# Kernel tuning notes

Measured on AMD Instinct MI355X. Metric: run time of the kernel, lower is better.

The kernel has to match this reference:

```python
import jax, jax.numpy as jnp
import numpy as np

NUM_HEADS = 12
NUM_GROUPS = 4
LN_EPS = 1e-12
NEG = -10000.0


def _ln(x, g, b):
    m = x.mean(-1, keepdims=True)
    v = ((x - m) ** 2).mean(-1, keepdims=True)
    return (x - m) * jax.lax.rsqrt(v + LN_EPS) * g + b


def _attention(h, ext_mask, Wattn, battn, ln):
    # h: [B,S,H]; ext_mask additive [B,1,1,S]; Wattn [4,H,H] = (q,k,v,o); battn [4,H]; ln [2,H]
    B, S, H = h.shape
    dh = H // NUM_HEADS
    q = (h @ Wattn[0] + battn[0]).reshape(B, S, NUM_HEADS, dh)
    k = (h @ Wattn[1] + battn[1]).reshape(B, S, NUM_HEADS, dh)
    v = (h @ Wattn[2] + battn[2]).reshape(B, S, NUM_HEADS, dh)
    scores = jnp.einsum('bqhd,bkhd->bhqk', q, k) * (1.0 / np.sqrt(dh)) + ext_mask
    p = jax.nn.softmax(scores, axis=-1)
    ctx = jnp.einsum('bhqk,bkhd->bqhd', p, v).reshape(B, S, H)
    # BertSelfOutput: dense + residual + LayerNorm
    return _ln(ctx @ Wattn[3] + battn[3] + h, ln[0], ln[1])


def _ffn(x, Wi, bi, Wo, bo, ln):
    # BertIntermediate (gelu) + BertOutput (dense + residual + LayerNorm)
    return _ln(jax.nn.gelu(x @ Wi + bi, approximate=False) @ Wo + bo + x, ln[0], ln[1])


def _bert_layer(h, ext_mask, Wattn, battn, ln_attn, Wi, bi, Wo, bo, ln_out):
    a = _attention(h, ext_mask, Wattn, battn, ln_attn)
    return _ffn(a, Wi, bi, Wo, bo, ln_out)


def _hier_attention(h, hier_mask, Wattn, battn, ln_attn, Wi, bi, Wo, bo, ln_out):
    # group masks [G,B,S]: 1 where hier_mask == group_id (ids 1..G)
    gids = jnp.arange(1, NUM_GROUPS + 1)
    masks = (hier_mask[None] == gids[:, None, None]).astype(h.dtype)  # [G,B,S]
    ext = (1.0 - masks)[:, :, None, None, :] * NEG                    # [G,B,1,1,S]
    # one full BertLayer per group (vectorized over G instead of batch concat)
    outs = jax.vmap(lambda m: _bert_layer(h, m, Wattn, battn, ln_attn, Wi, bi, Wo, bo, ln_out))(ext)  # [G,B,S,H]
    return jnp.sum(outs * masks[..., None], axis=0)


def reference(hidden_states, attention_mask, main_Wattn, main_battn, main_ln_attn,
              main_Wi, main_bi, main_Wo, main_bo, main_ln_out,
              hier_Wattn, hier_battn, hier_ln_attn, hier_Wi, hier_bi, hier_Wo,
              hier_bo, hier_ln_out, hier_mask):
    attn_out = _attention(hidden_states, attention_mask, main_Wattn, main_battn, main_ln_attn)
    hier_out = _hier_attention(hidden_states, hier_mask, hier_Wattn, hier_battn,
                               hier_ln_attn, hier_Wi, hier_bi, hier_Wo, hier_bo, hier_ln_out)
    combined = attn_out + hier_out
    return _ffn(combined, main_Wi, main_bi, main_Wo, main_bo, main_ln_out)


def setup_inputs() -> dict:
    key = jax.random.key(0)
    ks = jax.random.split(key, 20)
    B, S, H, F = 8, 512, 768, 3072
    W = 0.02  # weight init scale

    def layer_params(k):
        kk = jax.random.split(k, 8)
        return dict(
            Wattn=jax.random.normal(kk[0], (4, H, H), jnp.float32) * W,
            battn=jax.random.normal(kk[1], (4, H), jnp.float32) * W,
            ln_attn=jnp.stack([1.0 + jax.random.normal(kk[2], (H,), jnp.float32) * W,
                               jax.random.normal(kk[3], (H,), jnp.float32) * W]),
            Wi=jax.random.normal(kk[4], (H, F), jnp.float32) * W,
            bi=jax.random.normal(kk[5], (F,), jnp.float32) * W,
            Wo=jax.random.normal(kk[6], (F, H), jnp.float32) * W,
            bo=jax.random.normal(kk[7], (H,), jnp.float32) * W,
            ln_out=jnp.stack([1.0 + jax.random.normal(kk[2], (H,), jnp.float32) * W,
                              jax.random.normal(kk[3], (H,), jnp.float32) * W]),
        )

    main = layer_params(ks[0])
    hier = layer_params(ks[1])
    inp = {
        'hidden_states': jax.random.normal(ks[2], (B, S, H), jnp.float32),
        'attention_mask': jnp.zeros((B, 1, 1, S), jnp.float32),
        'hier_mask': jax.random.randint(ks[3], (B, S), 0, 5).astype(jnp.int64),
    }
    for name, p in (('main', main), ('hier', hier)):
        for k2, v in p.items():
            inp[f'{name}_{k2}'] = v
    return inp
```

## Files before the change

kernel.cpp:

```cpp
#include <hip/hip_runtime.h>
#include <hip/hip_bf16.h>

#define DI __device__ __forceinline__

typedef __attribute__((ext_vector_type(4))) float  f32x4;
typedef __attribute__((ext_vector_type(8))) short  s16x8;
typedef __attribute__((ext_vector_type(4))) short  s16x4;
typedef __attribute__((ext_vector_type(8))) __bf16 bf16x8;

DI short f2bf(float f) {
  union { float f; unsigned u; } v; v.f = f;
  unsigned r = v.u + 0x7fffu + ((v.u >> 16) & 1u);
  return (short)(r >> 16);
}

DI f32x4 mfma16(s16x8 a, s16x8 b, f32x4 c) {
  return __builtin_amdgcn_mfma_f32_16x16x32_bf16(
      __builtin_bit_cast(bf16x8, a), __builtin_bit_cast(bf16x8, b), c, 0, 0, 0);
}

typedef const __attribute__((address_space(1))) unsigned* gas_p;
typedef __attribute__((address_space(3))) unsigned* las_p;
DI void gload16(const void* g, void* l) {
  __builtin_amdgcn_global_load_lds((gas_p)g, (las_p)l, 16, 0, 0);
}

template<int N> DI void wait_vmcnt() {
  asm volatile("s_waitcnt vmcnt(%0)" :: "n"(N) : "memory");
}

__global__ __launch_bounds__(256) void cast_bf16(const float* __restrict__ x,
                                                 short* __restrict__ y) {
  const int i = (blockIdx.x * 256 + threadIdx.x) * 4;
  const float4 t = *(const float4*)&x[i];
  s16x4 o;
  o[0] = f2bf(t.x); o[1] = f2bf(t.y); o[2] = f2bf(t.z); o[3] = f2bf(t.w);
  *(s16x4*)&y[i] = o;
}

struct TJob { const float* src; short* dst; int K, N, tile0; };
struct TJobs { TJob j[12]; };

__global__ __launch_bounds__(256) void transpose_w(TJobs jobs) {
  __shared__ float T[32][33];
  const int t = blockIdx.x;
  int ji = 0;
#pragma unroll
  for (int i = 1; i < 12; ++i) if (jobs.j[i].tile0 <= t) ji = i;
  const float* src = jobs.j[ji].src;
  short* dst = jobs.j[ji].dst;
  const int K = jobs.j[ji].K, N = jobs.j[ji].N;
  const int lt = t - jobs.j[ji].tile0;
  const int tn = N >> 5;
  const int n0 = (lt % tn) << 5, k0 = (lt / tn) << 5;
  const int tid = threadIdx.x;
#pragma unroll
  for (int i = 0; i < 4; ++i) {
    const int c = i * 256 + tid, r = c >> 5, cc = c & 31;
    T[cc][r] = src[(long long)(k0 + r) * N + n0 + cc];
  }
  __syncthreads();
#pragma unroll
  for (int i = 0; i < 4; ++i) {
    const int c = i * 256 + tid, r = c >> 5, cc = c & 31;
    dst[(long long)(n0 + r) * K + k0 + cc] = f2bf(T[r][cc]);
  }
}

template<int BM, int BN, int WM, int WN, int EPI>
__global__ __launch_bounds__(256) void gemm_bt(
    const short* __restrict__ A, int lda, long long sA,
    const short* __restrict__ B, int ldb, long long sB,
    void* __restrict__ Cv, int ldc,
    long long cOuter, int cInner, int cStride,
    const float* __restrict__ bias,
    int K, int nSplit,
    short* __restrict__ vtOut) {
  constexpr int BK = 32;
  constexpr int WNW = BN / WN;
  constexpr int MFR = WM / 16, NFR = WN / 16;
  constexpr int ALD = BM / 64;
  constexpr int BLD = BN / 64;
  constexpr int LPT = ALD + BLD;

  __shared__ short As[3][BM * BK];
  __shared__ short Bs[3][BN * BK];

  const int z = blockIdx.z;
  const int zb = z / nSplit, zs = z - zb * nSplit;
  const short* Ab = A + (long long)zb * sA + (long long)zs * K;
  const short* Bb = B + (long long)zb * sB + (long long)zs * K;
  const long long cOff = (long long)(z / cInner) * cOuter + (long long)(z % cInner) * cStride;

  const int bm = blockIdx.x * BM;
  const int bn = blockIdx.y * BN;
  const int tid = threadIdx.x;
  const int wave = tid >> 6, lane = tid & 63;
  const int wm = (wave / WNW) * WM;
  const int wn = (wave % WNW) * WN;
  const int l16 = lane & 15, lk = lane >> 4;

  const int scol = ((tid & 3) ^ ((tid >> 3) & 3)) * 8;
  const short* aBase = Ab + (long long)(bm + (tid >> 2)) * lda + scol;
  const short* bBase = Bb + (long long)(bn + (tid >> 2)) * ldb + scol;
  const int ldsOff = wave * 64 * 8;
  const int rslot = (lk ^ ((l16 >> 1) & 3)) * 8;

  f32x4 acc[MFR][NFR] = {};

  auto stage = [&](int buf, int kt) {
#pragma unroll
    for (int i = 0; i < ALD; ++i)
      gload16(aBase + kt + (long long)(i * 64) * lda, &As[buf][i * 2048 + ldsOff]);
#pragma unroll
    for (int i = 0; i < BLD; ++i)
      gload16(bBase + kt + (long long)(i * 64) * ldb, &Bs[buf][i * 2048 + ldsOff]);
  };

  const int nt = K / BK;
  stage(0, 0);
  if (nt > 1) stage(1, BK);
  int cur = 0;
  for (int t = 0; t < nt; ++t) {
    if (t + 1 < nt) wait_vmcnt<LPT>();
    else            wait_vmcnt<0>();
    __builtin_amdgcn_s_barrier();
    s16x8 af[MFR], bfr[NFR];
#pragma unroll
    for (int mi = 0; mi < MFR; ++mi)
      af[mi] = *(const s16x8*)&As[cur][(wm + mi * 16 + l16) * BK + rslot];
#pragma unroll
    for (int ni = 0; ni < NFR; ++ni)
      bfr[ni] = *(const s16x8*)&Bs[cur][(wn + ni * 16 + l16) * BK + rslot];
#pragma unroll
    for (int mi = 0; mi < MFR; ++mi)
#pragma unroll
      for (int ni = 0; ni < NFR; ++ni)
        acc[mi][ni] = mfma16(bfr[ni], af[mi], acc[mi][ni]);
    if (t + 2 < nt) {
      const int nb = cur + 2 >= 3 ? cur - 1 : cur + 2;
      stage(nb, (t + 2) * BK);
    }
    cur = (cur + 1 == 3) ? 0 : cur + 1;
  }

#pragma unroll
  for (int mi = 0; mi < MFR; ++mi) {
    const int row = bm + wm + mi * 16 + l16;
#pragma unroll
    for (int ni = 0; ni < NFR; ++ni) {
      const int col = bn + wn + ni * 16 + lk * 4;
      const long long idx = cOff + (long long)row * ldc + col;
      f32x4 bv = {};
      if (EPI != 2 && bias) bv = *(const f32x4*)&bias[col];
      f32x4 v = acc[mi][ni] + bv;
      if constexpr (EPI == 0 || EPI == 3) {
        s16x4 o;
#pragma unroll
        for (int r = 0; r < 4; ++r) o[r] = f2bf(v[r]);
        *(s16x4*)&((short*)Cv)[idx] = o;
        if constexpr (EPI == 3) {
          if (col >= 1536) {
            const int b = row >> 9, s = row & 511;
            const int hc = col - 1536;
            const int bh = b * 12 + (hc >> 6);
            const int d0 = hc & 63;
            short* vp = vtOut + (long long)bh * 32768 + (long long)d0 * 512 + s;
#pragma unroll
            for (int r = 0; r < 4; ++r) vp[r * 512] = o[r];
          }
        }
      } else if constexpr (EPI == 1) {
        s16x4 o;
#pragma unroll
        for (int r = 0; r < 4; ++r) {
          const float g = 0.5f * v[r] * (1.f + erff(v[r] * 0.70710678118654752f));
          o[r] = f2bf(g);
        }
        *(s16x4*)&((short*)Cv)[idx] = o;
      } else {
        *(f32x4*)&((float*)Cv)[idx] = v;
      }
    }
  }
}

template<int HIER>
__global__ __launch_bounds__(256) void attn_scores(
    const short* __restrict__ QKV,
    const float* __restrict__ amask,
    const int* __restrict__ hmask,
    short* __restrict__ P) {
  __shared__ short Qs[32 * 64];
  __shared__ short Ks[256 * 64];
  __shared__ float red[32 * 4];
  __shared__ int   hm[512];

  const int bh = blockIdx.y;
  const int b = bh / 12, hh = bh % 12;
  const int q0 = blockIdx.x * 32;
  const int tid = threadIdx.x;
  const int wave = tid >> 6, lane = tid & 63;
  const int l16 = lane & 15, lk = lane >> 4;
  const long long rowbase = (long long)(b * 512) * 2304 + hh * 64;

  {
    const int c = tid;
    const int d8 = ((c & 7) ^ ((c >> 3) & 7)) * 8;
    gload16(QKV + rowbase + (long long)(q0 + (c >> 3)) * 2304 + d8,
            &Qs[wave * 64 * 8]);
  }
  if constexpr (HIER) {
    for (int i = tid; i < 512; i += 256) hm[i] = hmask[b * 512 + i];
  }

  f32x4 acc[2][8] = {};
#pragma unroll
  for (int kc = 0; kc < 2; ++kc) {
    if (kc) __syncthreads();
#pragma unroll
    for (int i = 0; i < 8; ++i) {
      const int c = i * 256 + tid;
      const int d8 = ((c & 7) ^ ((c >> 3) & 7)) * 8;
      gload16(QKV + rowbase + 768 + (long long)(kc * 256 + (c >> 3)) * 2304 + d8,
              &Ks[(i * 256 + wave * 64) * 8]);
    }
    __syncthreads();
#pragma unroll
    for (int ks = 0; ks < 2; ++ks) {
      s16x8 af[2], bfr[4];
#pragma unroll
      for (int mi = 0; mi < 2; ++mi)
        af[mi] = *(const s16x8*)&Qs[(mi * 16 + l16) * 64 +
                                    (((ks * 4 + lk) ^ (l16 & 7)) * 8)];
#pragma unroll
      for (int ni = 0; ni < 4; ++ni)
        bfr[ni] = *(const s16x8*)&Ks[(wave * 64 + ni * 16 + l16) * 64 +
                                     (((ks * 4 + lk) ^ (l16 & 7)) * 8)];
#pragma unroll
      for (int mi = 0; mi < 2; ++mi)
#pragma unroll
        for (int ni = 0; ni < 4; ++ni)
          acc[mi][kc * 4 + ni] = mfma16(af[mi], bfr[ni], acc[mi][kc * 4 + ni]);
    }
  }

  int gq[2][4];
  if constexpr (HIER) {
#pragma unroll
    for (int mi = 0; mi < 2; ++mi)
#pragma unroll
      for (int r = 0; r < 4; ++r)
        gq[mi][r] = hm[q0 + mi * 16 + lk * 4 + r];
  }
  int hk[8]; float am[8];
#pragma unroll
  for (int nig = 0; nig < 8; ++nig) {
    const int col = (nig >> 2) * 256 + wave * 64 + (nig & 3) * 16 + l16;
    if constexpr (HIER) hk[nig] = hm[col];
    else                am[nig] = amask[b * 512 + col];
  }
#pragma unroll
  for (int mi = 0; mi < 2; ++mi)
#pragma unroll
    for (int nig = 0; nig < 8; ++nig)
#pragma unroll
      for (int r = 0; r < 4; ++r) {
        float v = acc[mi][nig][r] * 0.125f;
        if constexpr (HIER) v += (hk[nig] == gq[mi][r]) ? 0.f : -10000.f;
        else                v += am[nig];
        acc[mi][nig][r] = v;
      }

  float mx[2][4];
#pragma unroll
  for (int mi = 0; mi < 2; ++mi)
#pragma unroll
    for (int r = 0; r < 4; ++r) {
      float m = acc[mi][0][r];
#pragma unroll
      for (int nig = 1; nig < 8; ++nig) m = fmaxf(m, acc[mi][nig][r]);
#pragma unroll
      for (int d = 1; d < 16; d <<= 1) m = fmaxf(m, __shfl_xor(m, d));
      mx[mi][r] = m;
      red[(mi * 16 + lk * 4 + r) * 4 + wave] = m;
    }
  __syncthreads();
#pragma unroll
  for (int mi = 0; mi < 2; ++mi)
#pragma unroll
    for (int r = 0; r < 4; ++r) {
      const int q = mi * 16 + lk * 4 + r;
      mx[mi][r] = fmaxf(fmaxf(red[q * 4], red[q * 4 + 1]),
                        fmaxf(red[q * 4 + 2], red[q * 4 + 3]));
    }
  __syncthreads();

  float sm[2][4];
#pragma unroll
  for (int mi = 0; mi < 2; ++mi)
#pragma unroll
    for (int r = 0; r < 4; ++r) {
      float s = 0.f;
#pragma unroll
      for (int nig = 0; nig < 8; ++nig) {
        const float e = __expf(acc[mi][nig][r] - mx[mi][r]);
        acc[mi][nig][r] = e;
        s += e;
      }
#pragma unroll
      for (int d = 1; d < 16; d <<= 1) s += __shfl_xor(s, d);
      sm[mi][r] = s;
      red[(mi * 16 + lk * 4 + r) * 4 + wave] = s;
    }
  __syncthreads();
#pragma unroll
  for (int mi = 0; mi < 2; ++mi)
#pragma unroll
    for (int r = 0; r < 4; ++r) {
      const int q = mi * 16 + lk * 4 + r;
      sm[mi][r] = 1.f / (red[q * 4] + red[q * 4 + 1] + red[q * 4 + 2] + red[q * 4 + 3]);
    }

  const long long Pbase = (long long)bh * 512 * 512;
#pragma unroll
  for (int mi = 0; mi < 2; ++mi)
#pragma unroll
    for (int nig = 0; nig < 8; ++nig) {
      const int col = (nig >> 2) * 256 + wave * 64 + (nig & 3) * 16 + l16;
#pragma unroll
      for (int r = 0; r < 4; ++r) {
        const int q = mi * 16 + lk * 4 + r;
        P[Pbase + (long long)(q0 + q) * 512 + col] = f2bf(acc[mi][nig][r] * sm[mi][r]);
      }
    }
}

template<int NS, int MODE>
__global__ __launch_bounds__(256) void ln_red(
    const float* __restrict__ part, const float* __restrict__ bias,
    const float* __restrict__ res, const float* __restrict__ ln,
    float* __restrict__ outf, short* __restrict__ outb,
    const int* __restrict__ hmask) {
  constexpr long long SP = 4096LL * 768;
  const int row = blockIdx.x * 4 + (threadIdx.x >> 6);
  const int lane = threadIdx.x & 63;
  const long long rb = (long long)row * 768;
  float v[12];
  float s = 0.f;
#pragma unroll
  for (int i = 0; i < 3; ++i) {
    const int c4 = lane + (i << 6);
    float4 t = ((const float4*)(res + rb))[c4];
    const float4 bv = ((const float4*)bias)[c4];
    t.x += bv.x; t.y += bv.y; t.z += bv.z; t.w += bv.w;
#pragma unroll
    for (int ss = 0; ss < NS; ++ss) {
      const float4 p = ((const float4*)(part + ss * SP + rb))[c4];
      t.x += p.x; t.y += p.y; t.z += p.z; t.w += p.w;
    }
    v[i * 4 + 0] = t.x; v[i * 4 + 1] = t.y; v[i * 4 + 2] = t.z; v[i * 4 + 3] = t.w;
    s += t.x + t.y + t.z + t.w;
  }
#pragma unroll
  for (int d = 1; d < 64; d <<= 1) s += __shfl_xor(s, d);
  const float mean = s * (1.f / 768.f);
  float vs = 0.f;
#pragma unroll
  for (int i = 0; i < 12; ++i) { const float dv = v[i] - mean; vs += dv * dv; }
#pragma unroll
  for (int d = 1; d < 64; d <<= 1) vs += __shfl_xor(vs, d);
  const float rstd = rsqrtf(vs * (1.f / 768.f) + 1e-12f);
  int keep = 1;
  if constexpr (MODE == 2) keep = (hmask[row] != 0);
#pragma unroll
  for (int i = 0; i < 3; ++i) {
    const int c4 = lane + (i << 6);
    const float4 g = ((const float4*)ln)[c4];
    const float4 be = ((const float4*)(ln + 768))[c4];
    const float gg[4] = {g.x, g.y, g.z, g.w}, bb[4] = {be.x, be.y, be.z, be.w};
    float resv[4];
#pragma unroll
    for (int j = 0; j < 4; ++j) {
      float yv = (v[i * 4 + j] - mean) * rstd * gg[j] + bb[j];
      if constexpr (MODE == 2) {
        const float a = outf[rb + c4 * 4 + j];
        yv = a + (keep ? yv : 0.f);
      }
      resv[j] = yv;
    }
    float4 of; of.x = resv[0]; of.y = resv[1]; of.z = resv[2]; of.w = resv[3];
    ((float4*)(outf + rb))[c4] = of;
    if constexpr (MODE >= 1) {
      s16x4 ob;
#pragma unroll
      for (int j = 0; j < 4; ++j) ob[j] = f2bf(resv[j]);
      *(s16x4*)&outb[rb + c4 * 4] = ob;
    }
  }
}

extern "C" void kernel_launch(void* const* d_in, const int* in_sizes, int n_in,
                              void* d_out, int out_size, void* d_ws, size_t ws_size,
                              hipStream_t stream) {
  (void)in_sizes; (void)n_in; (void)out_size; (void)ws_size;
  const float* h      = (const float*)d_in[0];
  const float* amask  = (const float*)d_in[1];
  const int*   hmask  = (const int*)d_in[2];
  const float* mWattn = (const float*)d_in[3];
  const float* mbattn = (const float*)d_in[4];
  const float* mlnA   = (const float*)d_in[5];
  const float* mWi    = (const float*)d_in[6];
  const float* mbi    = (const float*)d_in[7];
  const float* mWo    = (const float*)d_in[8];
  const float* mbo    = (const float*)d_in[9];
  const float* mlnO   = (const float*)d_in[10];
  const float* hWattn = (const float*)d_in[11];
  const float* hbattn = (const float*)d_in[12];
  const float* hlnA   = (const float*)d_in[13];
  const float* hWi    = (const float*)d_in[14];
  const float* hbi    = (const float*)d_in[15];
  const float* hWo    = (const float*)d_in[16];
  const float* hbo    = (const float*)d_in[17];
  const float* hlnO   = (const float*)d_in[18];
  float* out = (float*)d_out;

  char* ws = (char*)d_ws;
  size_t off = 0;
  auto alloc = [&](size_t bytes) {
    void* p = ws + off;
    off += (bytes + 255) & ~(size_t)255;
    return p;
  };
  short* wq_m = (short*)alloc(2304ull * 768 * 2);
  short* wq_h = (short*)alloc(2304ull * 768 * 2);
  short* wo2  = (short*)alloc(2ull * 768 * 768 * 2);
  short* wi_m = (short*)alloc(3072ull * 768 * 2);
  short* wi_h = (short*)alloc(3072ull * 768 * 2);
  short* wf_m = (short*)alloc(768ull * 3072 * 2);
  short* wf_h = (short*)alloc(768ull * 3072 * 2);
  short* hbf  = (short*)alloc(4096ull * 768 * 2);
  short* qkv  = (short*)alloc(4096ull * 2304 * 2);
  short* vt   = (short*)alloc(96ull * 64 * 512 * 2);
  short* Pb   = (short*)alloc(96ull * 512 * 512 * 2);
  short* ctxb = (short*)alloc(2ull * 4096 * 768 * 2);
  float* pre1 = (float*)alloc(4096ull * 768 * 4);
  float* attn = (float*)alloc(4096ull * 768 * 4);
  short* abf  = (short*)alloc(4096ull * 768 * 2);
  short* cbf  = (short*)alloc(4096ull * 768 * 2);
  short* mid  = qkv;
  float* part = (float*)Pb;

  const long long SC = 4096LL * 768;

  cast_bf16<<<dim3(3072), dim3(256), 0, stream>>>(h, hbf);

  TJobs tj; int tile = 0; int nj = 0;
  auto add = [&](const float* s, short* d, int K, int N) {
    tj.j[nj].src = s; tj.j[nj].dst = d; tj.j[nj].K = K; tj.j[nj].N = N; tj.j[nj].tile0 = tile;
    tile += (K / 32) * (N / 32); nj++;
  };
  add(mWattn,              wq_m,              768, 768);
  add(mWattn + 589824,     wq_m + 589824,     768, 768);
  add(mWattn + 2 * 589824, wq_m + 2 * 589824, 768, 768);
  add(mWattn + 3 * 589824, wo2,               768, 768);
  add(mWi,                 wi_m,              768, 3072);
  add(mWo,                 wf_m,              3072, 768);
  add(hWattn,              wq_h,              768, 768);
  add(hWattn + 589824,     wq_h + 589824,     768, 768);
  add(hWattn + 2 * 589824, wq_h + 2 * 589824, 768, 768);
  add(hWattn + 3 * 589824, wo2 + 589824,      768, 768);
  add(hWi,                 wi_h,              768, 3072);
  add(hWo,                 wf_h,              3072, 768);
  transpose_w<<<dim3(tile), dim3(256), 0, stream>>>(tj);

  auto attn_path = [&](const short* wq, const float* battn, int hier, short* ctx) {
    gemm_bt<128, 128, 64, 64, 3><<<dim3(32, 18, 1), dim3(256), 0, stream>>>(
        hbf, 768, 0, wq, 768, 0, qkv, 2304, 0, 1, 0, battn, 768, 1, vt);
    if (hier)
      attn_scores<1><<<dim3(16, 96), dim3(256), 0, stream>>>(qkv, amask, hmask, Pb);
    else
      attn_scores<0><<<dim3(16, 96), dim3(256), 0, stream>>>(qkv, amask, hmask, Pb);
    gemm_bt<64, 64, 32, 32, 0><<<dim3(8, 1, 96), dim3(256), 0, stream>>>(
        Pb, 512, 262144LL, vt, 512, 32768LL,
        ctx, 768, 512LL * 768, 12, 64, nullptr, 512, 1, nullptr);
  };

  attn_path(wq_m, mbattn, 0, ctxb);
  attn_path(wq_h, hbattn, 1, ctxb + SC);

  gemm_bt<128, 128, 64, 64, 2><<<dim3(32, 6, 4), dim3(256), 0, stream>>>(
      ctxb, 768, SC, wo2, 768, 589824LL, part, 768, SC, 1, 0, nullptr, 384, 2, nullptr);
  ln_red<2, 0><<<dim3(1024), dim3(256), 0, stream>>>(
      part, mbattn + 2304, h, mlnA, attn, nullptr, nullptr);
  ln_red<2, 1><<<dim3(1024), dim3(256), 0, stream>>>(
      part + 2 * SC, hbattn + 2304, h, hlnA, pre1, abf, nullptr);

  gemm_bt<128, 128, 64, 64, 1><<<dim3(32, 24, 1), dim3(256), 0, stream>>>(
      abf, 768, 0, wi_h, 768, 0, mid, 3072, 0, 1, 0, hbi, 768, 1, nullptr);
  gemm_bt<128, 128, 64, 64, 2><<<dim3(32, 6, 4), dim3(256), 0, stream>>>(
      mid, 3072, 0, wf_h, 3072, 0, part, 768, SC, 1, 0, nullptr, 768, 4, nullptr);
  ln_red<4, 2><<<dim3(1024), dim3(256), 0, stream>>>(
      part, hbo, pre1, hlnO, attn, cbf, hmask);

  gemm_bt<128, 128, 64, 64, 1><<<dim3(32, 24, 1), dim3(256), 0, stream>>>(
      cbf, 768, 0, wi_m, 768, 0, mid, 3072, 0, 1, 0, mbi, 768, 1, nullptr);
  gemm_bt<128, 128, 64, 64, 2><<<dim3(32, 6, 4), dim3(256), 0, stream>>>(
      mid, 3072, 0, wf_m, 3072, 0, part, 768, SC, 1, 0, nullptr, 768, 4, nullptr);
  ln_red<4, 0><<<dim3(1024), dim3(256), 0, stream>>>(
      part, mbo, attn, mlnO, out, nullptr, nullptr);
}
```

Measured before the change: 372.3 us.

## Add 2-wave 128x128 GEMM kernel and batch main/hier QKV projections

Adds a new 128-thread GEMM kernel where each of two waves computes a 64x128 sub-tile with double-buffered LDS. It is used for all large projections (QKV, output, FFN up and down) in place of the 256-thread triple-buffered kernel. The main and hierarchical QKV projections are also merged into one batched launch over a z dimension, with per-batch bias selection and a V-transpose output offset. The aim is more register-level reuse per wave and fewer launches, at the cost of higher register pressure, fewer threads per block and a shallower prefetch pipeline.

Result: slower. 525.0 us (+41.0%).

```diff
diff --git a/kernel.cpp b/kernel.cpp
--- a/kernel.cpp
+++ b/kernel.cpp
@@ -67,6 +67,115 @@
   }
 }
 
+template<int EPI>
+__global__ __launch_bounds__(128) void gemm2w(
+    const short* __restrict__ A, int lda, long long sA,
+    const short* __restrict__ B, int ldb, long long sB,
+    void* __restrict__ Cv, int ldc,
+    long long cOuter, int cInner, int cStride,
+    const float* __restrict__ bias, const float* __restrict__ bias2,
+    int K, int nSplit,
+    short* __restrict__ vtOut) {
+  constexpr int BK = 32;
+  __shared__ short As[2][128 * BK];
+  __shared__ short Bs[2][128 * BK];
+
+  const int z = blockIdx.z;
+  const int zb = z / nSplit, zs = z - zb * nSplit;
+  const short* Ab = A + (long long)zb * sA + (long long)zs * K;
+  const short* Bb = B + (long long)zb * sB + (long long)zs * K;
+  const long long cOff = (long long)(z / cInner) * cOuter + (long long)(z % cInner) * cStride;
+  const float* bi = (bias2 && zb) ? bias2 : bias;
+
+  const int bm = blockIdx.x * 128;
+  const int bn = blockIdx.y * 128;
+  const int tid = threadIdx.x;
+  const int wave = tid >> 6, lane = tid & 63;
+  const int l16 = lane & 15, lk = lane >> 4;
+
+  const int scol = ((tid & 3) ^ ((tid >> 3) & 3)) * 8;
+  const short* aBase = Ab + (long long)(bm + (tid >> 2)) * lda + scol;
+  const short* bBase = Bb + (long long)(bn + (tid >> 2)) * ldb + scol;
+  const int ldsOff = wave * 512;
+  const int rslot = (lk ^ ((l16 >> 1) & 3)) * 8;
+
+  f32x4 acc[4][8] = {};
+
+  auto stage = [&](int buf, int kt) {
+#pragma unroll
+    for (int i = 0; i < 4; ++i)
+      gload16(aBase + kt + (long long)(i * 32) * lda, &As[buf][i * 1024 + ldsOff]);
+#pragma unroll
+    for (int i = 0; i < 4; ++i)
+      gload16(bBase + kt + (long long)(i * 32) * ldb, &Bs[buf][i * 1024 + ldsOff]);
+  };
+
+  const int nt = K / BK;
+  stage(0, 0);
+  wait_vmcnt<0>();
+  __builtin_amdgcn_s_barrier();
+  int cur = 0;
+  for (int t = 0; t < nt; ++t) {
+    if (t + 1 < nt) stage(cur ^ 1, (t + 1) * BK);
+    s16x8 af[4], bfr[8];
+#pragma unroll
+    for (int mi = 0; mi < 4; ++mi)
+      af[mi] = *(const s16x8*)&As[cur][(wave * 64 + mi * 16 + l16) * BK + rslot];
+#pragma unroll
+    for (int ni = 0; ni < 8; ++ni)
+      bfr[ni] = *(const s16x8*)&Bs[cur][(ni * 16 + l16) * BK + rslot];
+#pragma unroll
+    for (int mi = 0; mi < 4; ++mi)
+#pragma unroll
+      for (int ni = 0; ni < 8; ++ni)
+        acc[mi][ni] = mfma16(bfr[ni], af[mi], acc[mi][ni]);
+    wait_vmcnt<0>();
+    __builtin_amdgcn_s_barrier();
+    cur ^= 1;
+  }
+
+#pragma unroll
+  for (int mi = 0; mi < 4; ++mi) {
+    const int row = bm + wave * 64 + mi * 16 + l16;
+#pragma unroll
+    for (int ni = 0; ni < 8; ++ni) {
+      const int col = bn + ni * 16 + lk * 4;
+      const long long idx = cOff + (long long)row * ldc + col;
+      f32x4 bv = {};
+      if (EPI != 2 && bi) bv = *(const f32x4*)&bi[col];
+      f32x4 v = acc[mi][ni] + bv;
+      if constexpr (EPI == 0 || EPI == 3) {
+        s16x4 o;
+#pragma unroll
+        for (int r = 0; r < 4; ++r) o[r] = f2bf(v[r]);
+        *(s16x4*)&((short*)Cv)[idx] = o;
+        if constexpr (EPI == 3) {
+          if (col >= 1536) {
+            const int b = row >> 9, s = row & 511;
+            const int hc = col - 1536;
+            const int bh = b * 12 + (hc >> 6);
+            const int d0 = hc & 63;
+            short* vp = vtOut + (long long)zb * 3145728 +
+                        (long long)bh * 32768 + (long long)d0 * 512 + s;
+#pragma unroll
+            for (int r = 0; r < 4; ++r) vp[r * 512] = o[r];
+          }
+        }
+      } else if constexpr (EPI == 1) {
+        s16x4 o;
+#pragma unroll
+        for (int r = 0; r < 4; ++r) {
+          const float g = 0.5f * v[r] * (1.f + erff(v[r] * 0.70710678118654752f));
+          o[r] = f2bf(g);
+        }
+        *(s16x4*)&((short*)Cv)[idx] = o;
+      } else {
+        *(f32x4*)&((float*)Cv)[idx] = v;
+      }
+    }
+  }
+}
+
 template<int BM, int BN, int WM, int WN, int EPI>
 __global__ __launch_bounds__(256) void gemm_bt(
     const short* __restrict__ A, int lda, long long sA,
@@ -74,8 +183,7 @@
     void* __restrict__ Cv, int ldc,
     long long cOuter, int cInner, int cStride,
     const float* __restrict__ bias,
-    int K, int nSplit,
-    short* __restrict__ vtOut) {
+    int K, int nSplit) {
   constexpr int BK = 32;
   constexpr int WNW = BN / WN;
   constexpr int MFR = WM / 16, NFR = WN / 16;
@@ -154,22 +262,11 @@
       f32x4 bv = {};
       if (EPI != 2 && bias) bv = *(const f32x4*)&bias[col];
       f32x4 v = acc[mi][ni] + bv;
-      if constexpr (EPI == 0 || EPI == 3) {
+      if constexpr (EPI == 0) {
         s16x4 o;
 #pragma unroll
         for (int r = 0; r < 4; ++r) o[r] = f2bf(v[r]);
         *(s16x4*)&((short*)Cv)[idx] = o;
-        if constexpr (EPI == 3) {
-          if (col >= 1536) {
-            const int b = row >> 9, s = row & 511;
-            const int hc = col - 1536;
-            const int bh = b * 12 + (hc >> 6);
-            const int d0 = hc & 63;
-            short* vp = vtOut + (long long)bh * 32768 + (long long)d0 * 512 + s;
-#pragma unroll
-            for (int r = 0; r < 4; ++r) vp[r * 512] = o[r];
-          }
-        }
       } else if constexpr (EPI == 1) {
         s16x4 o;
 #pragma unroll
@@ -432,26 +529,25 @@
     off += (bytes + 255) & ~(size_t)255;
     return p;
   };
-  short* wq_m = (short*)alloc(2304ull * 768 * 2);
-  short* wq_h = (short*)alloc(2304ull * 768 * 2);
+  const long long SC  = 4096LL * 768;
+  const long long SC3 = 4096LL * 2304;
+  short* wq2  = (short*)alloc(2ull * 2304 * 768 * 2);
   short* wo2  = (short*)alloc(2ull * 768 * 768 * 2);
   short* wi_m = (short*)alloc(3072ull * 768 * 2);
   short* wi_h = (short*)alloc(3072ull * 768 * 2);
   short* wf_m = (short*)alloc(768ull * 3072 * 2);
   short* wf_h = (short*)alloc(768ull * 3072 * 2);
   short* hbf  = (short*)alloc(4096ull * 768 * 2);
-  short* qkv  = (short*)alloc(4096ull * 2304 * 2);
-  short* vt   = (short*)alloc(96ull * 64 * 512 * 2);
+  short* qkv2 = (short*)alloc(2ull * SC3 * 2);
+  short* vt2  = (short*)alloc(2ull * 96 * 64 * 512 * 2);
   short* Pb   = (short*)alloc(96ull * 512 * 512 * 2);
   short* ctxb = (short*)alloc(2ull * 4096 * 768 * 2);
   float* pre1 = (float*)alloc(4096ull * 768 * 4);
   float* attn = (float*)alloc(4096ull * 768 * 4);
   short* abf  = (short*)alloc(4096ull * 768 * 2);
   short* cbf  = (short*)alloc(4096ull * 768 * 2);
-  short* mid  = qkv;
+  short* mid  = qkv2;
   float* part = (float*)Pb;
-
-  const long long SC = 4096LL * 768;
 
   cast_bf16<<<dim3(3072), dim3(256), 0, stream>>>(h, hbf);
 
@@ -460,53 +556,58 @@
     tj.j[nj].src = s; tj.j[nj].dst = d; tj.j[nj].K = K; tj.j[nj].N = N; tj.j[nj].tile0 = tile;
     tile += (K / 32) * (N / 32); nj++;
   };
-  add(mWattn,              wq_m,              768, 768);
-  add(mWattn + 589824,     wq_m + 589824,     768, 768);
-  add(mWattn + 2 * 589824, wq_m + 2 * 589824, 768, 768);
-  add(mWattn + 3 * 589824, wo2,               768, 768);
-  add(mWi,                 wi_m,              768, 3072);
-  add(mWo,                 wf_m,              3072, 768);
-  add(hWattn,              wq_h,              768, 768);
-  add(hWattn + 589824,     wq_h + 589824,     768, 768);
-  add(hWattn + 2 * 589824, wq_h + 2 * 589824, 768, 768);
-  add(hWattn + 3 * 589824, wo2 + 589824,      768, 768);
-  add(hWi,                 wi_h,              768, 3072);
-  add(hWo,                 wf_h,              3072, 768);
+  const long long WQ = 2304LL * 768;
+  add(mWattn,              wq2,                768, 768);
+  add(mWattn + 589824,     wq2 + 589824,       768, 768);
+  add(mWattn + 2 * 589824, wq2 + 2 * 589824,   768, 768);
+  add(mWattn + 3 * 589824, wo2,                768, 768);
+  add(mWi,                 wi_m,               768, 3072);
+  add(mWo,                 wf_m,               3072, 768);
+  add(hWattn,              wq2 + WQ,           768, 768);
+  add(hWattn + 589824,     wq2 + WQ + 589824,  768, 768);
+  add(hWattn + 2 * 589824, wq2 + WQ + 2 * 589824, 768, 768);
+  add(hWattn + 3 * 589824, wo2 + 589824,       768, 768);
+  add(hWi,                 wi_h,               768, 3072);
+  add(hWo,                 wf_h,               3072, 768);
   transpose_w<<<dim3(tile), dim3(256), 0, stream>>>(tj);
 
-  auto attn_path = [&](const short* wq, const float* battn, int hier, short* ctx) {
-    gemm_bt<128, 128, 64, 64, 3><<<dim3(32, 18, 1), dim3(256), 0, stream>>>(
-        hbf, 768, 0, wq, 768, 0, qkv, 2304, 0, 1, 0, battn, 768, 1, vt);
+  gemm2w<3><<<dim3(32, 18, 2), dim3(128), 0, stream>>>(
+      hbf, 768, 0, wq2, 768, WQ, qkv2, 2304, SC3, 1, 0,
+      mbattn, hbattn, 768, 1, vt2);
+
+  auto attn_tail = [&](int hier, short* ctx) {
+    const short* qkv = qkv2 + (long long)hier * SC3;
+    const short* vt  = vt2 + (long long)hier * 3145728;
     if (hier)
       attn_scores<1><<<dim3(16, 96), dim3(256), 0, stream>>>(qkv, amask, hmask, Pb);
     else
       attn_scores<0><<<dim3(16, 96), dim3(256), 0, stream>>>(qkv, amask, hmask, Pb);
     gemm_bt<64, 64, 32, 32, 0><<<dim3(8, 1, 96), dim3(256), 0, stream>>>(
         Pb, 512, 262144LL, vt, 512, 32768LL,
-        ctx, 768, 512LL * 768, 12, 64, nullptr, 512, 1, nullptr);
+        ctx, 768, 512LL * 768, 12, 64, nullptr, 512, 1);
   };
-
-  attn_path(wq_m, mbattn, 0, ctxb);
-  attn_path(wq_h, hbattn, 1, ctxb + SC);
-
-  gemm_bt<128, 128, 64, 64, 2><<<dim3(32, 6, 4), dim3(256), 0, stream>>>(
-      ctxb, 768, SC, wo2, 768, 589824LL, part, 768, SC, 1, 0, nullptr, 384, 2, nullptr);
+  attn_tail(0, ctxb);
+  attn_tail(1, ctxb + SC);
+
+  gemm2w<2><<<dim3(32, 6, 4), dim3(128), 0, stream>>>(
+      ctxb, 768, SC, wo2, 768, 589824LL, part, 768, SC, 1, 0,
+      nullptr, nullptr, 384, 2, nullptr);
   ln_red<2, 0><<<dim3(1024), dim3(256), 0, stream>>>(
       part, mbattn + 2304, h, mlnA, attn, nullptr, nullptr);
   ln_red<2, 1><<<dim3(1024), dim3(256), 0, stream>>>(
       part + 2 * SC, hbattn + 2304, h, hlnA, pre1, abf, nullptr);
 
-  gemm_bt<128, 128, 64, 64, 1><<<dim3(32, 24, 1), dim3(256), 0, stream>>>(
-      abf, 768, 0, wi_h, 768, 0, mid, 3072, 0, 1, 0, hbi, 768, 1, nullptr);
-  gemm_bt<128, 128, 64, 64, 2><<<dim3(32, 6, 4), dim3(256), 0, stream>>>(
-      mid, 3072, 0, wf_h, 3072, 0, part, 768, SC, 1, 0, nullptr, 768, 4, nullptr);
+  gemm2w<1><<<dim3(32, 24, 1), dim3(128), 0, stream>>>(
+      abf, 768, 0, wi_h, 768, 0, mid, 3072, 0, 1, 0, hbi, nullptr, 768, 1, nullptr);
+  gemm2w<2><<<dim3(32, 6, 4), dim3(128), 0, stream>>>(
+      mid, 3072, 0, wf_h, 3072, 0, part, 768, SC, 1, 0, nullptr, nullptr, 768, 4, nullptr);
   ln_red<4, 2><<<dim3(1024), dim3(256), 0, stream>>>(
       part, hbo, pre1, hlnO, attn, cbf, hmask);
 
-  gemm_bt<128, 128, 64, 64, 1><<<dim3(32, 24, 1), dim3(256), 0, stream>>>(
-      cbf, 768, 0, wi_m, 768, 0, mid, 3072, 0, 1, 0, mbi, 768, 1, nullptr);
-  gemm_bt<128, 128, 64, 64, 2><<<dim3(32, 6, 4), dim3(256), 0, stream>>>(
-      mid, 3072, 0, wf_m, 3072, 0, part, 768, SC, 1, 0, nullptr, 768, 4, nullptr);
+  gemm2w<1><<<dim3(32, 24, 1), dim3(128), 0, stream>>>(
+      cbf, 768, 0, wi_m, 768, 0, mid, 3072, 0, 1, 0, mbi, nullptr, 768, 1, nullptr);
+  gemm2w<2><<<dim3(32, 6, 4), dim3(128), 0, stream>>>(
+      mid, 3072, 0, wf_m, 3072, 0, part, 768, SC, 1, 0, nullptr, nullptr, 768, 4, nullptr);
   ln_red<4, 0><<<dim3(1024), dim3(256), 0, stream>>>(
       part, mbo, attn, mlnO, out, nullptr, nullptr);
 }
```
